# Kernel tuning notes

Hardware: AMD Instinct MI355X
Metric: run time of the kernel (lower is better)

Reference implementation:

```python
import math
import jax, jax.numpy as jnp
import numpy as np
from jax import lax

N = 224
EPS_BN = 1e-5


def _conv(x, w, b):
    y = lax.conv_general_dilated(x, w, (1, 1), 'SAME',
                                 dimension_numbers=('NCHW', 'OIHW', 'NCHW'))
    return y + b[None, :, None, None]


def _bn(x, g, beta, m, v):
    # eval-mode BatchNorm2d with running stats
    inv = lax.rsqrt(v + EPS_BN)
    return (x - m[None, :, None, None]) * (g * inv)[None, :, None, None] + beta[None, :, None, None]


def _maxpool2(x):
    return lax.reduce_window(x, -jnp.inf, lax.max, (1, 1, 2, 2), (1, 1, 2, 2), 'VALID')


def setup_inputs() -> dict:
    key = jax.random.key(0)
    ks = jax.random.split(key, 12)
    idx = np.arange(N, dtype=np.float32)
    angles = 2.0 * math.pi * idx[None, :] * idx[:, None] / N
    inp = {
        'sequences': jax.random.normal(ks[0], (16, 8, 3, N, N), dtype=jnp.float32),
        'dft_cos': jnp.asarray(np.cos(angles), dtype=jnp.float32),
        'dft_sin': jnp.asarray(np.sin(angles), dtype=jnp.float32),
        'conv1_w': jax.random.normal(ks[1], (16, 3, 3, 3), dtype=jnp.float32) * 0.1,
        'conv1_b': jnp.zeros((16,), jnp.float32),
        'bn1_g': jnp.ones((16,), jnp.float32),
        'bn1_b': jnp.zeros((16,), jnp.float32),
        'bn1_m': jnp.zeros((16,), jnp.float32),
        'bn1_v': jnp.ones((16,), jnp.float32),
        'conv2_w': jax.random.normal(ks[2], (32, 16, 3, 3), dtype=jnp.float32) * 0.05,
        'conv2_b': jnp.zeros((32,), jnp.float32),
        'bn2_g': jnp.ones((32,), jnp.float32),
        'bn2_b': jnp.zeros((32,), jnp.float32),
        'bn2_m': jnp.zeros((32,), jnp.float32),
        'bn2_v': jnp.ones((32,), jnp.float32),
        'conv3_w': jax.random.normal(ks[3], (64, 32, 3, 3), dtype=jnp.float32) * 0.05,
        'conv3_b': jnp.zeros((64,), jnp.float32),
        'bn3_g': jnp.ones((64,), jnp.float32),
        'bn3_b': jnp.zeros((64,), jnp.float32),
        'bn3_m': jnp.zeros((64,), jnp.float32),
        'bn3_v': jnp.ones((64,), jnp.float32),
        'fc_w': jax.random.normal(ks[4], (128, 64), dtype=jnp.float32) * 0.1,
        'fc_b': jnp.zeros((128,), jnp.float32),
    }
    return inp


def reference(sequences, dft_cos, dft_sin,
              conv1_w, conv1_b, bn1_g, bn1_b, bn1_m, bn1_v,
              conv2_w, conv2_b, bn2_g, bn2_b, bn2_m, bn2_v,
              conv3_w, conv3_b, bn3_g, bn3_b, bn3_m, bn3_v,
              fc_w, fc_b):
    b, s = sequences.shape[0], sequences.shape[1]
    x = sequences[:, s // 2]  # center frames [B,3,H,W]

    # 2D DFT via dense matmul chain: X = (C - jS) x (C - jS)
    C, S = dft_cos, dft_sin
    Cx = jnp.einsum('ij,bcjk->bcik', C, x)
    Sx = jnp.einsum('ij,bcjk->bcik', S, x)
    X_real = jnp.einsum('bcij,jk->bcik', Cx, C) - jnp.einsum('bcij,jk->bcik', Sx, S)
    X_imag = -(jnp.einsum('bcij,jk->bcik', Cx, S) + jnp.einsum('bcij,jk->bcik', Sx, C))
    magnitude = jnp.sqrt(X_real ** 2 + X_imag ** 2 + 1e-08)
    spec = jnp.log(magnitude + 1e-08)
    half = N // 2
    spec = jnp.roll(spec, shift=(half, half), axis=(-2, -1))  # fftshift

    # CNN stack (eval-mode BN, dropout disabled)
    h = jax.nn.relu(_bn(_conv(spec, conv1_w, conv1_b), bn1_g, bn1_b, bn1_m, bn1_v))
    h = _maxpool2(h)
    h = jax.nn.relu(_bn(_conv(h, conv2_w, conv2_b), bn2_g, bn2_b, bn2_m, bn2_v))
    h = _maxpool2(h)
    h = jax.nn.relu(_bn(_conv(h, conv3_w, conv3_b), bn3_g, bn3_b, bn3_m, bn3_v))
    h = jnp.mean(h, axis=(2, 3))  # AdaptiveAvgPool2d((1,1)) + flatten -> [B,64]

    freq_out = jax.nn.relu(h @ fc_w.T + fc_b)  # dropout = identity in eval
    return freq_out
```

## Files before the change

kernel.cpp:

```cpp
#include <hip/hip_runtime.h>
#include <math.h>
#include <stddef.h>

#define N224 224
#define PIX 50176
#define ROWS113 25312

#define OFF_SX    1214976
#define OFF_SPEC  4816896
#define OFF_WT    3211264
#define OFF_WT2   (OFF_WT + 18432)
#define OFF_WT1   (OFF_WT + 23040)
#define OFF_SU3   (OFF_WT + 23472)
#define OFF_SU2   (OFF_WT + 23600)
#define OFF_SU1   (OFF_WT + 23664)
#define OFF_PART  (OFF_WT + 32768)

__global__ __launch_bounds__(256) void prep(
    const float* __restrict__ c1w, const float* __restrict__ c2w,
    const float* __restrict__ c3w, const float* __restrict__ c1b,
    const float* __restrict__ c2b, const float* __restrict__ c3b,
    const float* __restrict__ g1, const float* __restrict__ be1,
    const float* __restrict__ m1, const float* __restrict__ v1,
    const float* __restrict__ g2, const float* __restrict__ be2,
    const float* __restrict__ m2, const float* __restrict__ v2,
    const float* __restrict__ g3, const float* __restrict__ be3,
    const float* __restrict__ m3, const float* __restrict__ v3,
    float* __restrict__ wt3, float* __restrict__ wt2, float* __restrict__ wt1,
    float* __restrict__ su3, float* __restrict__ su2, float* __restrict__ su1)
{
  const int idx = blockIdx.x * 256 + threadIdx.x;
  const int stride = gridDim.x * 256;
  for (int i = idx; i < 18432; i += stride) {
    const int co = i & 63, k = (i >> 6) % 9, cc = i / 576;
    wt3[i] = c3w[co*288 + cc*9 + k];
  }
  for (int i = idx; i < 4608; i += stride) {
    const int co = i & 31, k = (i >> 5) % 9, cc = i / 288;
    wt2[i] = c2w[co*144 + cc*9 + k];
  }
  for (int i = idx; i < 432; i += stride) {
    const int co = i & 15, k = (i >> 4) % 9, cc = i / 144;
    wt1[i] = c1w[co*27 + cc*9 + k];
  }
  if (idx < 64) {
    const float s = g3[idx] * rsqrtf(v3[idx] + 1e-5f);
    su3[idx] = s; su3[64+idx] = (c3b[idx] - m3[idx]) * s + be3[idx];
  } else if (idx < 96) {
    const int c = idx - 64;
    const float s = g2[c] * rsqrtf(v2[c] + 1e-5f);
    su2[c] = s; su2[32+c] = (c2b[c] - m2[c]) * s + be2[c];
  } else if (idx < 112) {
    const int c = idx - 96;
    const float s = g1[c] * rsqrtf(v1[c] + 1e-5f);
    su1[c] = s; su1[16+c] = (c1b[c] - m1[c]) * s + be1[c];
  }
}

__global__ __launch_bounds__(64) void dft1(
    const float* __restrict__ seq, const float* __restrict__ Cm,
    const float* __restrict__ Sm, float* __restrict__ Cx, float* __restrict__ Sx)
{
  const int p = blockIdx.z;
  const int b = p / 3, ch = p % 3;
  const float* __restrict__ x = seq + ((((size_t)b * 8 + 4) * 3 + ch) * PIX);
  const int i0 = blockIdx.y * 32;
  const int k0 = blockIdx.x * 32;
  const int tid = threadIdx.x;
  const int tx = tid & 7, ty = tid >> 3;
  __shared__ float Ctt[16][36], Stt[16][36], Xt[16][36];
  float aC[4][4], aS[4][4];
#pragma unroll
  for (int a = 0; a < 4; ++a)
#pragma unroll
    for (int d = 0; d < 4; ++d) { aC[a][d] = 0.f; aS[a][d] = 0.f; }

  const int sr = tid >> 1;
  const int sk = (tid & 1) * 8;
  const int xj = tid >> 2;
  const int xk = (tid & 3) * 8;

  const float* xbase = x  + (size_t)xj * N224 + k0 + xk;
  const float* cbase = Cm + (size_t)(i0 + sr) * N224 + sk;
  const float* sbase = Sm + (size_t)(i0 + sr) * N224 + sk;

  float4 rx0 = *(const float4*)(xbase);
  float4 rx1 = *(const float4*)(xbase + 4);
  float4 rc0 = *(const float4*)(cbase);
  float4 rc1 = *(const float4*)(cbase + 4);
  float4 rs0 = *(const float4*)(sbase);
  float4 rs1 = *(const float4*)(sbase + 4);

  for (int jt = 0; jt < 14; ++jt) {
    __syncthreads();
    *(float4*)&Xt[xj][xk]     = rx0;
    *(float4*)&Xt[xj][xk + 4] = rx1;
    Ctt[sk+0][sr]=rc0.x; Ctt[sk+1][sr]=rc0.y; Ctt[sk+2][sr]=rc0.z; Ctt[sk+3][sr]=rc0.w;
    Ctt[sk+4][sr]=rc1.x; Ctt[sk+5][sr]=rc1.y; Ctt[sk+6][sr]=rc1.z; Ctt[sk+7][sr]=rc1.w;
    Stt[sk+0][sr]=rs0.x; Stt[sk+1][sr]=rs0.y; Stt[sk+2][sr]=rs0.z; Stt[sk+3][sr]=rs0.w;
    Stt[sk+4][sr]=rs1.x; Stt[sk+5][sr]=rs1.y; Stt[sk+6][sr]=rs1.z; Stt[sk+7][sr]=rs1.w;
    __syncthreads();
    if (jt < 13) {
      const int j = (jt + 1) * 16;
      rx0 = *(const float4*)(xbase + (size_t)j * N224);
      rx1 = *(const float4*)(xbase + (size_t)j * N224 + 4);
      rc0 = *(const float4*)(cbase + j);
      rc1 = *(const float4*)(cbase + j + 4);
      rs0 = *(const float4*)(sbase + j);
      rs1 = *(const float4*)(sbase + j + 4);
    }
#pragma unroll
    for (int jj = 0; jj < 16; ++jj) {
      const float4 cv4 = *(const float4*)&Ctt[jj][4*ty];
      const float4 sv4 = *(const float4*)&Stt[jj][4*ty];
      const float4 xv4 = *(const float4*)&Xt[jj][4*tx];
      const float cva[4] = {cv4.x, cv4.y, cv4.z, cv4.w};
      const float sva[4] = {sv4.x, sv4.y, sv4.z, sv4.w};
      const float xva[4] = {xv4.x, xv4.y, xv4.z, xv4.w};
#pragma unroll
      for (int a = 0; a < 4; ++a)
#pragma unroll
        for (int d = 0; d < 4; ++d) {
          aC[a][d] = fmaf(cva[a], xva[d], aC[a][d]);
          aS[a][d] = fmaf(sva[a], xva[d], aS[a][d]);
        }
    }
  }
  const size_t b113 = (size_t)p * ROWS113;
#pragma unroll
  for (int a = 0; a < 4; ++a) {
    const int i = i0 + 4*ty + a;
    if (i <= 112) {
      const size_t off = b113 + (size_t)i * N224 + k0 + 4*tx;
      *(float4*)&Cx[off] = make_float4(aC[a][0], aC[a][1], aC[a][2], aC[a][3]);
      *(float4*)&Sx[off] = make_float4(aS[a][0], aS[a][1], aS[a][2], aS[a][3]);
    }
  }
}

__global__ __launch_bounds__(64) void dft2(
    const float* __restrict__ Cx, const float* __restrict__ Sx,
    const float* __restrict__ Cm, const float* __restrict__ Sm,
    float* __restrict__ spec)
{
  const int p = blockIdx.z;
  const int i0 = blockIdx.y * 32;
  const int k0 = blockIdx.x * 32;
  const int tid = threadIdx.x;
  const int tx = tid & 7, ty = tid >> 3;
  const size_t b113 = (size_t)p * ROWS113;
  __shared__ float CxT[16][36], SxT[16][36], Ct[16][36], St[16][36];
  float p1[4][4], p2[4][4], p3[4][4], p4[4][4];
#pragma unroll
  for (int a = 0; a < 4; ++a)
#pragma unroll
    for (int d = 0; d < 4; ++d) { p1[a][d]=0.f; p2[a][d]=0.f; p3[a][d]=0.f; p4[a][d]=0.f; }

  const int sr = tid >> 1;
  const int sk = (tid & 1) * 8;
  const int ri = (i0 + sr > 112) ? 112 : i0 + sr;
  const int xj = tid >> 2;
  const int xk = (tid & 3) * 8;

  const float* cxb = Cx + b113 + (size_t)ri * N224 + sk;
  const float* sxb = Sx + b113 + (size_t)ri * N224 + sk;
  const float* ccb = Cm + (size_t)xj * N224 + k0 + xk;
  const float* ssb = Sm + (size_t)xj * N224 + k0 + xk;

  float4 ra0 = *(const float4*)(cxb);
  float4 ra1 = *(const float4*)(cxb + 4);
  float4 rb0 = *(const float4*)(sxb);
  float4 rb1 = *(const float4*)(sxb + 4);
  float4 rc0 = *(const float4*)(ccb);
  float4 rc1 = *(const float4*)(ccb + 4);
  float4 rd0 = *(const float4*)(ssb);
  float4 rd1 = *(const float4*)(ssb + 4);

  for (int jt = 0; jt < 14; ++jt) {
    __syncthreads();
    *(float4*)&Ct[xj][xk]     = rc0;  *(float4*)&Ct[xj][xk + 4] = rc1;
    *(float4*)&St[xj][xk]     = rd0;  *(float4*)&St[xj][xk + 4] = rd1;
    CxT[sk+0][sr]=ra0.x; CxT[sk+1][sr]=ra0.y; CxT[sk+2][sr]=ra0.z; CxT[sk+3][sr]=ra0.w;
    CxT[sk+4][sr]=ra1.x; CxT[sk+5][sr]=ra1.y; CxT[sk+6][sr]=ra1.z; CxT[sk+7][sr]=ra1.w;
    SxT[sk+0][sr]=rb0.x; SxT[sk+1][sr]=rb0.y; SxT[sk+2][sr]=rb0.z; SxT[sk+3][sr]=rb0.w;
    SxT[sk+4][sr]=rb1.x; SxT[sk+5][sr]=rb1.y; SxT[sk+6][sr]=rb1.z; SxT[sk+7][sr]=rb1.w;
    __syncthreads();
    if (jt < 13) {
      const int j = (jt + 1) * 16;
      ra0 = *(const float4*)(cxb + j);
      ra1 = *(const float4*)(cxb + j + 4);
      rb0 = *(const float4*)(sxb + j);
      rb1 = *(const float4*)(sxb + j + 4);
      rc0 = *(const float4*)(ccb + (size_t)j * N224);
      rc1 = *(const float4*)(ccb + (size_t)j * N224 + 4);
      rd0 = *(const float4*)(ssb + (size_t)j * N224);
      rd1 = *(const float4*)(ssb + (size_t)j * N224 + 4);
    }
#pragma unroll
    for (int jj = 0; jj < 16; ++jj) {
      const float4 cx4 = *(const float4*)&CxT[jj][4*ty];
      const float4 sx4 = *(const float4*)&SxT[jj][4*ty];
      const float4 cc4 = *(const float4*)&Ct[jj][4*tx];
      const float4 ss4 = *(const float4*)&St[jj][4*tx];
      const float cxa[4] = {cx4.x, cx4.y, cx4.z, cx4.w};
      const float sxa[4] = {sx4.x, sx4.y, sx4.z, sx4.w};
      const float cca[4] = {cc4.x, cc4.y, cc4.z, cc4.w};
      const float ssa[4] = {ss4.x, ss4.y, ss4.z, ss4.w};
#pragma unroll
      for (int a = 0; a < 4; ++a)
#pragma unroll
        for (int d = 0; d < 4; ++d) {
          p1[a][d] = fmaf(cxa[a], cca[d], p1[a][d]);
          p2[a][d] = fmaf(sxa[a], ssa[d], p2[a][d]);
          p3[a][d] = fmaf(cxa[a], ssa[d], p3[a][d]);
          p4[a][d] = fmaf(sxa[a], cca[d], p4[a][d]);
        }
    }
  }
  const size_t sb = (size_t)p * PIX;
  const int kk0 = k0 + 4*tx;
  const int ok0 = (kk0 < 112) ? kk0 + 112 : kk0 - 112;
#pragma unroll
  for (int a = 0; a < 4; ++a) {
    const int i = i0 + 4*ty + a;
    if (i > 112) continue;
    float sp1[4], sp2[4];
#pragma unroll
    for (int d = 0; d < 4; ++d) {
      const float re = p1[a][d] - p2[a][d];
      const float im = p3[a][d] + p4[a][d];
      sp1[d] = logf(sqrtf(fmaf(re, re, fmaf(im, im, 1e-8f))) + 1e-8f);
      const float re2 = p1[a][d] + p2[a][d];
      const float im2 = p3[a][d] - p4[a][d];
      sp2[d] = logf(sqrtf(fmaf(re2, re2, fmaf(im2, im2, 1e-8f))) + 1e-8f);
    }
    const int oi = (i < 112) ? i + 112 : i - 112;
    *(float4*)&spec[sb + (size_t)oi * N224 + ok0] =
        make_float4(sp1[0], sp1[1], sp1[2], sp1[3]);
    if (i >= 1 && i <= 111)
      *(float4*)&spec[sb + (size_t)(112 - i) * N224 + ok0] =
          make_float4(sp2[0], sp2[1], sp2[2], sp2[3]);
  }
}

__global__ __launch_bounds__(256) void conv1(
    const float* __restrict__ spec, const float* __restrict__ wt1,
    const float* __restrict__ su1, float* __restrict__ out)
{
  const int band = blockIdx.x, b = blockIdx.y;
  const int tid = threadIdx.x;
  const int w = tid >> 6, lane = tid & 63;
  const int co = lane & 15, xsub = lane >> 4;
  __shared__ float in_t[3][6][232];
  for (int i = tid; i < 3*6*232; i += 256) {
    const int c = i % 232, j = (i / 232) % 6, cc = i / 1392;
    const int y = band*4 - 1 + j, gx = c - 1;
    float v = 0.f;
    if (c < 226 && y >= 0 && y < 224 && gx >= 0 && gx < 224)
      v = spec[((size_t)b*3 + cc) * PIX + (size_t)y * N224 + gx];
    in_t[cc][j][c] = v;
  }
  __syncthreads();
  const int pr = w >> 1, xh = w & 1;
  const int X0 = xh*112 + xsub*28;
  const int jb = 2*pr;
  float acc[2][28];
#pragma unroll
  for (int r = 0; r < 2; ++r)
#pragma unroll
    for (int px = 0; px < 28; ++px) acc[r][px] = 0.f;
#pragma unroll
  for (int cc = 0; cc < 3; ++cc) {
    float wr[9];
#pragma unroll
    for (int k = 0; k < 9; ++k) wr[k] = wt1[(cc*9 + k)*16 + co];
#pragma unroll
    for (int rr = 0; rr < 4; ++rr) {
      float xr[32];
      const float4* rp = (const float4*)&in_t[cc][jb+rr][X0];
#pragma unroll
      for (int t = 0; t < 8; ++t) {
        const float4 v = rp[t];
        xr[4*t]=v.x; xr[4*t+1]=v.y; xr[4*t+2]=v.z; xr[4*t+3]=v.w;
      }
#pragma unroll
      for (int cr = 0; cr < 2; ++cr) {
        const int ky = rr - cr;
        if (ky < 0 || ky > 2) continue;
#pragma unroll
        for (int px = 0; px < 28; ++px) {
          acc[cr][px] = fmaf(xr[px  ], wr[ky*3  ], acc[cr][px]);
          acc[cr][px] = fmaf(xr[px+1], wr[ky*3+1], acc[cr][px]);
          acc[cr][px] = fmaf(xr[px+2], wr[ky*3+2], acc[cr][px]);
        }
      }
    }
  }
  const float s = su1[co], u = su1[16+co];
  const int py = band*2 + pr, pxb = X0 >> 1;
#pragma unroll
  for (int p = 0; p < 14; ++p) {
    const float v0 = acc[0][2*p]*s + u,   v1 = acc[0][2*p+1]*s + u;
    const float v2 = acc[1][2*p]*s + u,   v3 = acc[1][2*p+1]*s + u;
    out[(((size_t)b*16 + co)*112 + py)*112 + pxb + p] =
        fmaxf(fmaxf(fmaxf(v0, v1), fmaxf(v2, v3)), 0.f);
  }
}

__global__ __launch_bounds__(256) void conv2(
    const float* __restrict__ h1, const float* __restrict__ wt2,
    const float* __restrict__ su2, float* __restrict__ out)
{
  const int band = blockIdx.x, b = blockIdx.y;
  const int tid = threadIdx.x;
  const int w = tid >> 6, lane = tid & 63;
  const int co = lane & 31, xsub = lane >> 5;
  __shared__ float in_t[16][6][120];
  for (int i = tid; i < 16*6*120; i += 256) {
    const int c = i % 120, j = (i / 120) % 6, cc = i / 720;
    const int y = band*4 - 1 + j, gx = c - 1;
    float v = 0.f;
    if (c < 114 && y >= 0 && y < 112 && gx >= 0 && gx < 112)
      v = h1[(((size_t)b*16 + cc)*112 + y)*112 + gx];
    in_t[cc][j][c] = v;
  }
  __syncthreads();
  const int pr = w >> 1, xh = w & 1;
  const int X0 = xh*56 + xsub*28;
  const int jb = 2*pr;
  float acc[2][28];
#pragma unroll
  for (int r = 0; r < 2; ++r)
#pragma unroll
    for (int px = 0; px < 28; ++px) acc[r][px] = 0.f;
  for (int cc = 0; cc < 16; ++cc) {
    float wr[9];
#pragma unroll
    for (int k = 0; k < 9; ++k) wr[k] = wt2[(cc*9 + k)*32 + co];
#pragma unroll
    for (int rr = 0; rr < 4; ++rr) {
      float xr[32];
      const float4* rp = (const float4*)&in_t[cc][jb+rr][X0];
#pragma unroll
      for (int t = 0; t < 8; ++t) {
        const float4 v = rp[t];
        xr[4*t]=v.x; xr[4*t+1]=v.y; xr[4*t+2]=v.z; xr[4*t+3]=v.w;
      }
#pragma unroll
      for (int cr = 0; cr < 2; ++cr) {
        const int ky = rr - cr;
        if (ky < 0 || ky > 2) continue;
#pragma unroll
        for (int px = 0; px < 28; ++px) {
          acc[cr][px] = fmaf(xr[px  ], wr[ky*3  ], acc[cr][px]);
          acc[cr][px] = fmaf(xr[px+1], wr[ky*3+1], acc[cr][px]);
          acc[cr][px] = fmaf(xr[px+2], wr[ky*3+2], acc[cr][px]);
        }
      }
    }
  }
  const float s = su2[co], u = su2[32+co];
  const int py = band*2 + pr, pxb = X0 >> 1;
#pragma unroll
  for (int p = 0; p < 14; ++p) {
    const float v0 = acc[0][2*p]*s + u,   v1 = acc[0][2*p+1]*s + u;
    const float v2 = acc[1][2*p]*s + u,   v3 = acc[1][2*p+1]*s + u;
    out[(((size_t)b*32 + co)*56 + py)*56 + pxb + p] =
        fmaxf(fmaxf(fmaxf(v0, v1), fmaxf(v2, v3)), 0.f);
  }
}

__global__ __launch_bounds__(256) void conv3(
    const float* __restrict__ h2, const float* __restrict__ wt3,
    const float* __restrict__ su3, float* __restrict__ part)
{
  const int band = blockIdx.x, b = blockIdx.y;
  const int tid = threadIdx.x;
  const int w = tid >> 6, co = tid & 63;
  __shared__ float in_t[32][4][60];
  for (int i = tid; i < 32*4*60; i += 256) {
    const int c = i % 60, j = (i / 60) % 4, cc = i / 240;
    const int y = band*2 - 1 + j, gx = c - 1;
    float v = 0.f;
    if (c < 58 && y >= 0 && y < 56 && gx >= 0 && gx < 56)
      v = h2[(((size_t)b*32 + cc)*56 + y)*56 + gx];
    in_t[cc][j][c] = v;
  }
  __syncthreads();
  const int rb = w >> 1, xh = w & 1;
  const int X0 = xh * 28;
  float acc[28];
#pragma unroll
  for (int px = 0; px < 28; ++px) acc[px] = 0.f;
  for (int cc = 0; cc < 32; ++cc) {
    float wr[9];
#pragma unroll
    for (int k = 0; k < 9; ++k) wr[k] = wt3[(cc*9 + k)*64 + co];
#pragma unroll
    for (int rr = 0; rr < 3; ++rr) {
      float xr[32];
      const float4* rp = (const float4*)&in_t[cc][rb+rr][X0];
#pragma unroll
      for (int t = 0; t < 8; ++t) {
        const float4 v = rp[t];
        xr[4*t]=v.x; xr[4*t+1]=v.y; xr[4*t+2]=v.z; xr[4*t+3]=v.w;
      }
#pragma unroll
      for (int px = 0; px < 28; ++px) {
        acc[px] = fmaf(xr[px  ], wr[rr*3  ], acc[px]);
        acc[px] = fmaf(xr[px+1], wr[rr*3+1], acc[px]);
        acc[px] = fmaf(xr[px+2], wr[rr*3+2], acc[px]);
      }
    }
  }
  const float s = su3[co], u = su3[64+co];
  float sum = 0.f;
#pragma unroll
  for (int px = 0; px < 28; ++px)
    sum += fmaxf(acc[px]*s + u, 0.f);
  part[((size_t)b*64 + co)*112 + band*4 + w] = sum;
}

__global__ __launch_bounds__(128) void mean_fc(
    const float* __restrict__ part, const float* __restrict__ fw,
    const float* __restrict__ fb, float* __restrict__ out)
{
  const int b = blockIdx.x;
  const int tid = threadIdx.x;
  __shared__ float h3s[64];
  if (tid < 64) {
    float s = 0.f;
    const float* pp = part + ((size_t)b*64 + tid)*112;
#pragma unroll
    for (int i = 0; i < 112; ++i) s += pp[i];
    h3s[tid] = s * (1.0f / 3136.0f);
  }
  __syncthreads();
  float acc = fb[tid];
#pragma unroll
  for (int c = 0; c < 64; ++c)
    acc = fmaf(h3s[c], fw[tid*64 + c], acc);
  out[b*128 + tid] = fmaxf(acc, 0.f);
}

extern "C" void kernel_launch(void* const* d_in, const int* in_sizes, int n_in,
                              void* d_out, int out_size, void* d_ws, size_t ws_size,
                              hipStream_t stream) {
  const float* seq  = (const float*)d_in[0];
  const float* dcos = (const float*)d_in[1];
  const float* dsin = (const float*)d_in[2];
  const float* c1w  = (const float*)d_in[3];
  const float* c1b  = (const float*)d_in[4];
  const float* b1g  = (const float*)d_in[5];
  const float* b1b  = (const float*)d_in[6];
  const float* b1m  = (const float*)d_in[7];
  const float* b1v  = (const float*)d_in[8];
  const float* c2w  = (const float*)d_in[9];
  const float* c2b  = (const float*)d_in[10];
  const float* b2g  = (const float*)d_in[11];
  const float* b2b  = (const float*)d_in[12];
  const float* b2m  = (const float*)d_in[13];
  const float* b2v  = (const float*)d_in[14];
  const float* c3w  = (const float*)d_in[15];
  const float* c3b  = (const float*)d_in[16];
  const float* b3g  = (const float*)d_in[17];
  const float* b3b  = (const float*)d_in[18];
  const float* b3m  = (const float*)d_in[19];
  const float* b3v  = (const float*)d_in[20];
  const float* fw   = (const float*)d_in[21];
  const float* fb   = (const float*)d_in[22];
  float* out = (float*)d_out;

  float* ws   = (float*)d_ws;
  float* Cx   = ws;
  float* Sx   = ws + OFF_SX;
  float* spec = ws + OFF_SPEC;
  float* h1   = ws;
  float* h2   = ws + OFF_SPEC;
  float* wt3  = ws + OFF_WT;
  float* wt2  = ws + OFF_WT2;
  float* wt1  = ws + OFF_WT1;
  float* su3  = ws + OFF_SU3;
  float* su2  = ws + OFF_SU2;
  float* su1  = ws + OFF_SU1;
  float* part = ws + OFF_PART;

  prep<<<24, 256, 0, stream>>>(c1w, c2w, c3w, c1b, c2b, c3b,
                               b1g, b1b, b1m, b1v, b2g, b2b, b2m, b2v,
                               b3g, b3b, b3m, b3v, wt3, wt2, wt1, su3, su2, su1);
  dft1<<<dim3(7, 4, 48), 64, 0, stream>>>(seq, dcos, dsin, Cx, Sx);
  dft2<<<dim3(7, 4, 48), 64, 0, stream>>>(Cx, Sx, dcos, dsin, spec);
  conv1<<<dim3(56, 16), 256, 0, stream>>>(spec, wt1, su1, h1);
  conv2<<<dim3(28, 16), 256, 0, stream>>>(h1, wt2, su2, h2);
  conv3<<<dim3(28, 16), 256, 0, stream>>>(h2, wt3, su3, part);
  mean_fc<<<16, 128, 0, stream>>>(part, fw, fb, out);
}
```

Measured before the change: 198.1 us.

## Use 256-thread blocks with 2x2 microtiles and exploit column symmetry in DFT

Both DFT kernels move from 64 threads with 4x4 register tiles to 256 threads with 2x2 tiles, which raises thread-level parallelism per block and removes the register prefetch double-buffering. The second DFT pass now also uses conjugate symmetry along the column axis, computing only columns up to 112 and writing four mirrored outputs per value, so its grid shrinks from 7 to 4 column blocks. This is meant to cut the work in the second matmul stage and improve occupancy. The cost is more shared-memory traffic per FMA, scalar scattered stores, and no overlap of global loads with compute.

```diff
diff --git a/kernel.cpp b/kernel.cpp
--- a/kernel.cpp
+++ b/kernel.cpp
@@ -57,7 +57,7 @@
   }
 }
 
-__global__ __launch_bounds__(64) void dft1(
+__global__ __launch_bounds__(256) void dft1(
     const float* __restrict__ seq, const float* __restrict__ Cm,
     const float* __restrict__ Sm, float* __restrict__ Cx, float* __restrict__ Sx)
 {
@@ -67,78 +67,54 @@
   const int i0 = blockIdx.y * 32;
   const int k0 = blockIdx.x * 32;
   const int tid = threadIdx.x;
-  const int tx = tid & 7, ty = tid >> 3;
+  const int tx = tid & 15, ty = tid >> 4;
   __shared__ float Ctt[16][36], Stt[16][36], Xt[16][36];
-  float aC[4][4], aS[4][4];
-#pragma unroll
-  for (int a = 0; a < 4; ++a)
-#pragma unroll
-    for (int d = 0; d < 4; ++d) { aC[a][d] = 0.f; aS[a][d] = 0.f; }
-
-  const int sr = tid >> 1;
-  const int sk = (tid & 1) * 8;
-  const int xj = tid >> 2;
-  const int xk = (tid & 3) * 8;
-
-  const float* xbase = x  + (size_t)xj * N224 + k0 + xk;
-  const float* cbase = Cm + (size_t)(i0 + sr) * N224 + sk;
-  const float* sbase = Sm + (size_t)(i0 + sr) * N224 + sk;
-
-  float4 rx0 = *(const float4*)(xbase);
-  float4 rx1 = *(const float4*)(xbase + 4);
-  float4 rc0 = *(const float4*)(cbase);
-  float4 rc1 = *(const float4*)(cbase + 4);
-  float4 rs0 = *(const float4*)(sbase);
-  float4 rs1 = *(const float4*)(sbase + 4);
+  float aC[2][2] = {{0,0},{0,0}}, aS[2][2] = {{0,0},{0,0}};
+
+  const int sidx = tid & 127;
+  const int srow = sidx >> 2;
+  const int skq  = (sidx & 3) * 4;
+  const bool isC = tid < 128;
+  const float* __restrict__ csb = (isC ? Cm : Sm) + (size_t)(i0 + srow) * N224 + skq;
+  const int xjr = tid >> 4;
+  const int xc  = (tid & 15) * 2;
+  const float* __restrict__ xb = x + (size_t)xjr * N224 + k0 + xc;
 
   for (int jt = 0; jt < 14; ++jt) {
+    const int j = jt * 16;
     __syncthreads();
-    *(float4*)&Xt[xj][xk]     = rx0;
-    *(float4*)&Xt[xj][xk + 4] = rx1;
-    Ctt[sk+0][sr]=rc0.x; Ctt[sk+1][sr]=rc0.y; Ctt[sk+2][sr]=rc0.z; Ctt[sk+3][sr]=rc0.w;
-    Ctt[sk+4][sr]=rc1.x; Ctt[sk+5][sr]=rc1.y; Ctt[sk+6][sr]=rc1.z; Ctt[sk+7][sr]=rc1.w;
-    Stt[sk+0][sr]=rs0.x; Stt[sk+1][sr]=rs0.y; Stt[sk+2][sr]=rs0.z; Stt[sk+3][sr]=rs0.w;
-    Stt[sk+4][sr]=rs1.x; Stt[sk+5][sr]=rs1.y; Stt[sk+6][sr]=rs1.z; Stt[sk+7][sr]=rs1.w;
+    {
+      const float4 v = *(const float4*)(csb + j);
+      float (*dst)[36] = isC ? Ctt : Stt;
+      dst[skq+0][srow] = v.x; dst[skq+1][srow] = v.y;
+      dst[skq+2][srow] = v.z; dst[skq+3][srow] = v.w;
+      *(float2*)&Xt[xjr][xc] = *(const float2*)(xb + (size_t)j * N224);
+    }
     __syncthreads();
-    if (jt < 13) {
-      const int j = (jt + 1) * 16;
-      rx0 = *(const float4*)(xbase + (size_t)j * N224);
-      rx1 = *(const float4*)(xbase + (size_t)j * N224 + 4);
-      rc0 = *(const float4*)(cbase + j);
-      rc1 = *(const float4*)(cbase + j + 4);
-      rs0 = *(const float4*)(sbase + j);
-      rs1 = *(const float4*)(sbase + j + 4);
-    }
 #pragma unroll
     for (int jj = 0; jj < 16; ++jj) {
-      const float4 cv4 = *(const float4*)&Ctt[jj][4*ty];
-      const float4 sv4 = *(const float4*)&Stt[jj][4*ty];
-      const float4 xv4 = *(const float4*)&Xt[jj][4*tx];
-      const float cva[4] = {cv4.x, cv4.y, cv4.z, cv4.w};
-      const float sva[4] = {sv4.x, sv4.y, sv4.z, sv4.w};
-      const float xva[4] = {xv4.x, xv4.y, xv4.z, xv4.w};
-#pragma unroll
-      for (int a = 0; a < 4; ++a)
-#pragma unroll
-        for (int d = 0; d < 4; ++d) {
-          aC[a][d] = fmaf(cva[a], xva[d], aC[a][d]);
-          aS[a][d] = fmaf(sva[a], xva[d], aS[a][d]);
-        }
+      const float2 cv = *(const float2*)&Ctt[jj][2*ty];
+      const float2 sv = *(const float2*)&Stt[jj][2*ty];
+      const float2 xv = *(const float2*)&Xt[jj][2*tx];
+      aC[0][0] = fmaf(cv.x, xv.x, aC[0][0]); aC[0][1] = fmaf(cv.x, xv.y, aC[0][1]);
+      aC[1][0] = fmaf(cv.y, xv.x, aC[1][0]); aC[1][1] = fmaf(cv.y, xv.y, aC[1][1]);
+      aS[0][0] = fmaf(sv.x, xv.x, aS[0][0]); aS[0][1] = fmaf(sv.x, xv.y, aS[0][1]);
+      aS[1][0] = fmaf(sv.y, xv.x, aS[1][0]); aS[1][1] = fmaf(sv.y, xv.y, aS[1][1]);
     }
   }
   const size_t b113 = (size_t)p * ROWS113;
 #pragma unroll
-  for (int a = 0; a < 4; ++a) {
-    const int i = i0 + 4*ty + a;
+  for (int a = 0; a < 2; ++a) {
+    const int i = i0 + 2*ty + a;
     if (i <= 112) {
-      const size_t off = b113 + (size_t)i * N224 + k0 + 4*tx;
-      *(float4*)&Cx[off] = make_float4(aC[a][0], aC[a][1], aC[a][2], aC[a][3]);
-      *(float4*)&Sx[off] = make_float4(aS[a][0], aS[a][1], aS[a][2], aS[a][3]);
-    }
-  }
-}
-
-__global__ __launch_bounds__(64) void dft2(
+      const size_t off = b113 + (size_t)i * N224 + k0 + 2*tx;
+      *(float2*)&Cx[off] = make_float2(aC[a][0], aC[a][1]);
+      *(float2*)&Sx[off] = make_float2(aS[a][0], aS[a][1]);
+    }
+  }
+}
+
+__global__ __launch_bounds__(256) void dft2(
     const float* __restrict__ Cx, const float* __restrict__ Sx,
     const float* __restrict__ Cm, const float* __restrict__ Sm,
     float* __restrict__ spec)
@@ -147,69 +123,49 @@
   const int i0 = blockIdx.y * 32;
   const int k0 = blockIdx.x * 32;
   const int tid = threadIdx.x;
-  const int tx = tid & 7, ty = tid >> 3;
+  const int tx = tid & 15, ty = tid >> 4;
   const size_t b113 = (size_t)p * ROWS113;
   __shared__ float CxT[16][36], SxT[16][36], Ct[16][36], St[16][36];
-  float p1[4][4], p2[4][4], p3[4][4], p4[4][4];
-#pragma unroll
-  for (int a = 0; a < 4; ++a)
-#pragma unroll
-    for (int d = 0; d < 4; ++d) { p1[a][d]=0.f; p2[a][d]=0.f; p3[a][d]=0.f; p4[a][d]=0.f; }
-
-  const int sr = tid >> 1;
-  const int sk = (tid & 1) * 8;
-  const int ri = (i0 + sr > 112) ? 112 : i0 + sr;
-  const int xj = tid >> 2;
-  const int xk = (tid & 3) * 8;
-
-  const float* cxb = Cx + b113 + (size_t)ri * N224 + sk;
-  const float* sxb = Sx + b113 + (size_t)ri * N224 + sk;
-  const float* ccb = Cm + (size_t)xj * N224 + k0 + xk;
-  const float* ssb = Sm + (size_t)xj * N224 + k0 + xk;
-
-  float4 ra0 = *(const float4*)(cxb);
-  float4 ra1 = *(const float4*)(cxb + 4);
-  float4 rb0 = *(const float4*)(sxb);
-  float4 rb1 = *(const float4*)(sxb + 4);
-  float4 rc0 = *(const float4*)(ccb);
-  float4 rc1 = *(const float4*)(ccb + 4);
-  float4 rd0 = *(const float4*)(ssb);
-  float4 rd1 = *(const float4*)(ssb + 4);
+  float p1[2][2] = {{0,0},{0,0}}, p2[2][2] = {{0,0},{0,0}};
+  float p3[2][2] = {{0,0},{0,0}}, p4[2][2] = {{0,0},{0,0}};
+
+  const int sidx = tid & 127;
+  const int srow = sidx >> 2;
+  const int skq  = (sidx & 3) * 4;
+  const bool isCx = tid < 128;
+  const int ri = (i0 + srow > 112) ? 112 : i0 + srow;
+  const float* __restrict__ ab = (isCx ? Cx : Sx) + b113 + (size_t)ri * N224 + skq;
+  const int jr = tid >> 4;
+  const int cc2 = (tid & 15) * 2;
+  const float* __restrict__ cb = Cm + (size_t)jr * N224 + k0 + cc2;
+  const float* __restrict__ sb2 = Sm + (size_t)jr * N224 + k0 + cc2;
 
   for (int jt = 0; jt < 14; ++jt) {
+    const int j = jt * 16;
     __syncthreads();
-    *(float4*)&Ct[xj][xk]     = rc0;  *(float4*)&Ct[xj][xk + 4] = rc1;
-    *(float4*)&St[xj][xk]     = rd0;  *(float4*)&St[xj][xk + 4] = rd1;
-    CxT[sk+0][sr]=ra0.x; CxT[sk+1][sr]=ra0.y; CxT[sk+2][sr]=ra0.z; CxT[sk+3][sr]=ra0.w;
-    CxT[sk+4][sr]=ra1.x; CxT[sk+5][sr]=ra1.y; CxT[sk+6][sr]=ra1.z; CxT[sk+7][sr]=ra1.w;
-    SxT[sk+0][sr]=rb0.x; SxT[sk+1][sr]=rb0.y; SxT[sk+2][sr]=rb0.z; SxT[sk+3][sr]=rb0.w;
-    SxT[sk+4][sr]=rb1.x; SxT[sk+5][sr]=rb1.y; SxT[sk+6][sr]=rb1.z; SxT[sk+7][sr]=rb1.w;
+    {
+      const float4 v = *(const float4*)(ab + j);
+      float (*dst)[36] = isCx ? CxT : SxT;
+      dst[skq+0][srow] = v.x; dst[skq+1][srow] = v.y;
+      dst[skq+2][srow] = v.z; dst[skq+3][srow] = v.w;
+      *(float2*)&Ct[jr][cc2] = *(const float2*)(cb + (size_t)j * N224);
+      *(float2*)&St[jr][cc2] = *(const float2*)(sb2 + (size_t)j * N224);
+    }
     __syncthreads();
-    if (jt < 13) {
-      const int j = (jt + 1) * 16;
-      ra0 = *(const float4*)(cxb + j);
-      ra1 = *(const float4*)(cxb + j + 4);
-      rb0 = *(const float4*)(sxb + j);
-      rb1 = *(const float4*)(sxb + j + 4);
-      rc0 = *(const float4*)(ccb + (size_t)j * N224);
-      rc1 = *(const float4*)(ccb + (size_t)j * N224 + 4);
-      rd0 = *(const float4*)(ssb + (size_t)j * N224);
-      rd1 = *(const float4*)(ssb + (size_t)j * N224 + 4);
-    }
 #pragma unroll
     for (int jj = 0; jj < 16; ++jj) {
-      const float4 cx4 = *(const float4*)&CxT[jj][4*ty];
-      const float4 sx4 = *(const float4*)&SxT[jj][4*ty];
-      const float4 cc4 = *(const float4*)&Ct[jj][4*tx];
-      const float4 ss4 = *(const float4*)&St[jj][4*tx];
-      const float cxa[4] = {cx4.x, cx4.y, cx4.z, cx4.w};
-      const float sxa[4] = {sx4.x, sx4.y, sx4.z, sx4.w};
-      const float cca[4] = {cc4.x, cc4.y, cc4.z, cc4.w};
-      const float ssa[4] = {ss4.x, ss4.y, ss4.z, ss4.w};
-#pragma unroll
-      for (int a = 0; a < 4; ++a)
-#pragma unroll
-        for (int d = 0; d < 4; ++d) {
+      const float2 cxv = *(const float2*)&CxT[jj][2*ty];
+      const float2 sxv = *(const float2*)&SxT[jj][2*ty];
+      const float2 ccv = *(const float2*)&Ct[jj][2*tx];
+      const float2 ssv = *(const float2*)&St[jj][2*tx];
+      const float cxa[2] = {cxv.x, cxv.y};
+      const float sxa[2] = {sxv.x, sxv.y};
+      const float cca[2] = {ccv.x, ccv.y};
+      const float ssa[2] = {ssv.x, ssv.y};
+#pragma unroll
+      for (int a = 0; a < 2; ++a)
+#pragma unroll
+        for (int d = 0; d < 2; ++d) {
           p1[a][d] = fmaf(cxa[a], cca[d], p1[a][d]);
           p2[a][d] = fmaf(sxa[a], ssa[d], p2[a][d]);
           p3[a][d] = fmaf(cxa[a], ssa[d], p3[a][d]);
@@ -218,28 +174,31 @@
     }
   }
   const size_t sb = (size_t)p * PIX;
-  const int kk0 = k0 + 4*tx;
-  const int ok0 = (kk0 < 112) ? kk0 + 112 : kk0 - 112;
-#pragma unroll
-  for (int a = 0; a < 4; ++a) {
-    const int i = i0 + 4*ty + a;
+#pragma unroll
+  for (int a = 0; a < 2; ++a) {
+    const int i = i0 + 2*ty + a;
     if (i > 112) continue;
-    float sp1[4], sp2[4];
-#pragma unroll
-    for (int d = 0; d < 4; ++d) {
-      const float re = p1[a][d] - p2[a][d];
-      const float im = p3[a][d] + p4[a][d];
-      sp1[d] = logf(sqrtf(fmaf(re, re, fmaf(im, im, 1e-8f))) + 1e-8f);
-      const float re2 = p1[a][d] + p2[a][d];
-      const float im2 = p3[a][d] - p4[a][d];
-      sp2[d] = logf(sqrtf(fmaf(re2, re2, fmaf(im2, im2, 1e-8f))) + 1e-8f);
-    }
-    const int oi = (i < 112) ? i + 112 : i - 112;
-    *(float4*)&spec[sb + (size_t)oi * N224 + ok0] =
-        make_float4(sp1[0], sp1[1], sp1[2], sp1[3]);
-    if (i >= 1 && i <= 111)
-      *(float4*)&spec[sb + (size_t)(112 - i) * N224 + ok0] =
-          make_float4(sp2[0], sp2[1], sp2[2], sp2[3]);
+    const int shi  = (i < 112) ? i + 112 : i - 112;
+    const int shmi = 112 - i;
+    const bool irm = (i >= 1) && (i <= 111);
+#pragma unroll
+    for (int d = 0; d < 2; ++d) {
+      const int k = k0 + 2*tx + d;
+      if (k > 112) continue;
+      const float r1 = p1[a][d] - p2[a][d];
+      const float i1 = p3[a][d] + p4[a][d];
+      const float sp1v = logf(sqrtf(fmaf(r1, r1, fmaf(i1, i1, 1e-8f))) + 1e-8f);
+      const float r2v = p1[a][d] + p2[a][d];
+      const float i2v = p3[a][d] - p4[a][d];
+      const float sp2v = logf(sqrtf(fmaf(r2v, r2v, fmaf(i2v, i2v, 1e-8f))) + 1e-8f);
+      const int shk  = (k < 112) ? k + 112 : k - 112;
+      const int shmk = 112 - k;
+      const bool krm = (k >= 1) && (k <= 111);
+      spec[sb + (size_t)shi*N224 + shk] = sp1v;
+      if (irm)        spec[sb + (size_t)shmi*N224 + shk ] = sp2v;
+      if (krm)        spec[sb + (size_t)shi *N224 + shmk] = sp2v;
+      if (irm && krm) spec[sb + (size_t)shmi*N224 + shmk] = sp1v;
+    }
   }
 }
 
@@ -488,8 +447,8 @@
   prep<<<24, 256, 0, stream>>>(c1w, c2w, c3w, c1b, c2b, c3b,
                                b1g, b1b, b1m, b1v, b2g, b2b, b2m, b2v,
                                b3g, b3b, b3m, b3v, wt3, wt2, wt1, su3, su2, su1);
-  dft1<<<dim3(7, 4, 48), 64, 0, stream>>>(seq, dcos, dsin, Cx, Sx);
-  dft2<<<dim3(7, 4, 48), 64, 0, stream>>>(Cx, Sx, dcos, dsin, spec);
+  dft1<<<dim3(7, 4, 48), 256, 0, stream>>>(seq, dcos, dsin, Cx, Sx);
+  dft2<<<dim3(4, 4, 48), 256, 0, stream>>>(Cx, Sx, dcos, dsin, spec);
   conv1<<<dim3(56, 16), 256, 0, stream>>>(spec, wt1, su1, h1);
   conv2<<<dim3(28, 16), 256, 0, stream>>>(h1, wt2, su2, h2);
   conv3<<<dim3(28, 16), 256, 0, stream>>>(h2, wt3, su3, part);
```

Result: faster. 191.3 us (-3.4%).
